# Performance work log

Measured on AMD Instinct MI355X. Metric: run time of the kernel, lower is better.

## Reference

```python
import jax, jax.numpy as jnp
import numpy as np
import math

B, S, D, H = 4, 2048, 768, 12
HD = D // H  # 64


def setup_inputs() -> dict:
    key = jax.random.key(0)
    ks = jax.random.split(key, 9)
    s = 0.02
    return {
        "hidden_states": jax.random.normal(ks[0], (B, S, D), jnp.float32),
        "layout_q": jax.random.normal(ks[1], (B, S, D), jnp.float32),
        "layout_k": jax.random.normal(ks[2], (B, S, D), jnp.float32),
        "attention_mask": jnp.zeros((B, 1, 1, S), jnp.float32),
        "Wq": jax.random.normal(ks[3], (D, D), jnp.float32) * s,
        "bq": jnp.zeros((D,), jnp.float32),
        "Wk": jax.random.normal(ks[4], (D, D), jnp.float32) * s,
        "bk": jnp.zeros((D,), jnp.float32),
        "Wv": jax.random.normal(ks[5], (D, D), jnp.float32) * s,
        "bv": jnp.zeros((D,), jnp.float32),
    }


def _split_heads(x):
    # [B,S,D] -> [B,H,S,HD]
    return x.reshape(B, S, H, HD).transpose(0, 2, 1, 3)


def reference(hidden_states, layout_q, layout_k, attention_mask, Wq, bq, Wk, bk, Wv, bv):
    q = _split_heads(hidden_states @ Wq.T + bq)
    k = _split_heads(hidden_states @ Wk.T + bk)
    v = _split_heads(hidden_states @ Wv.T + bv)
    lq = _split_heads(layout_q)
    lk = _split_heads(layout_k)
    scale = 1.0 / math.sqrt(HD)
    # dual-stream scores: content + layout, both [B,H,S,S]
    scores = (jnp.einsum("bhqd,bhkd->bhqk", q, k)
              + jnp.einsum("bhqd,bhkd->bhqk", lq, lk)) * scale
    scores = scores + attention_mask
    probs = jax.nn.softmax(scores, axis=-1)
    ctx = jnp.einsum("bhqk,bhkd->bhqd", probs, v)
    return ctx.transpose(0, 2, 1, 3).reshape(B, S, D)
```

## Files before the change

kernel.cpp:

```cpp
#include <hip/hip_runtime.h>


typedef __attribute__((ext_vector_type(8))) short short8;
typedef __attribute__((ext_vector_type(4))) float floatx4;

#define LOG2E 1.4426950408889634f
#define QSCL 0.18033688011112042f

static constexpr int Sn = 2048, Dn = 768, Hn = 12, BHn = 48;

__device__ __forceinline__ unsigned short f2bf(float f) {
  unsigned u = __float_as_uint(f);
  u += 0x7FFFu + ((u >> 16) & 1u);
  return (unsigned short)(u >> 16);
}

__device__ __forceinline__ unsigned pack2bf(float lo, float hi) {
  return (unsigned)f2bf(lo) | ((unsigned)f2bf(hi) << 16);
}

typedef const __attribute__((address_space(1))) unsigned int* gas_t;
typedef __attribute__((address_space(3))) unsigned int* las_t;
__device__ __forceinline__ void async16(const void* g, void* l) {
  __builtin_amdgcn_global_load_lds((gas_t)g, (las_t)l, 16, 0, 0);
}

__global__ void cast_hs_kernel(const float* __restrict__ in, unsigned short* __restrict__ out, int n4) {
  int i = blockIdx.x * 256 + threadIdx.x;
  if (i >= n4) return;
  float4 v = ((const float4*)in)[i];
  ushort4 o = make_ushort4(f2bf(v.x), f2bf(v.y), f2bf(v.z), f2bf(v.w));
  ((ushort4*)out)[i] = o;
}

__global__ void cast_w_kernel(const float* __restrict__ w0, const float* __restrict__ w1,
                              const float* __restrict__ w2, unsigned short* __restrict__ out) {
  int i = blockIdx.x * 256 + threadIdx.x;
  const float* src = (blockIdx.y == 0) ? w0 : (blockIdx.y == 1) ? w1 : w2;
  float4 v = ((const float4*)src)[i];
  ushort4 o = make_ushort4(f2bf(v.x), f2bf(v.y), f2bf(v.z), f2bf(v.w));
  ((ushort4*)(out + (size_t)blockIdx.y * Dn * Dn))[i] = o;
}

__global__ void pack_layout_kernel(const float* __restrict__ lq, const float* __restrict__ lk,
                                   unsigned short* __restrict__ Qc, unsigned short* __restrict__ Kc) {
  int idx = blockIdx.x * 256 + threadIdx.x;
  const float* src = blockIdx.y ? lk : lq;
  unsigned short* dst = blockIdx.y ? Kc : Qc;
  const float sc = blockIdx.y ? 1.0f : QSCL;
  int d8 = idx & 7;
  int tt = idx >> 3;
  int h = tt % Hn;
  int bs = tt / Hn;
  int b = bs >> 11, s = bs & (Sn - 1);
  float4 v0 = ((const float4*)src)[idx * 2];
  float4 v1 = ((const float4*)src)[idx * 2 + 1];
  short8 o;
  o[0] = (short)f2bf(v0.x * sc); o[1] = (short)f2bf(v0.y * sc);
  o[2] = (short)f2bf(v0.z * sc); o[3] = (short)f2bf(v0.w * sc);
  o[4] = (short)f2bf(v1.x * sc); o[5] = (short)f2bf(v1.y * sc);
  o[6] = (short)f2bf(v1.z * sc); o[7] = (short)f2bf(v1.w * sc);
  size_t off = ((size_t)(b * Hn + h) * Sn + s) * 128 + 64 + d8 * 8;
  *(short8*)(dst + off) = o;
}

__global__ __launch_bounds__(256, 3)
void proj_kernel(const unsigned short* __restrict__ X,
                 const unsigned short* __restrict__ Wb,
                 const float* __restrict__ bq, const float* __restrict__ bk, const float* __restrict__ bv,
                 unsigned short* __restrict__ Qc, unsigned short* __restrict__ Kc,
                 unsigned short* __restrict__ Vt) {
  __shared__ __align__(16) unsigned short sMem[16384];
  unsigned short* const sA = sMem;
  unsigned short* const sB = sMem + 8192;

  const int z = blockIdx.z;
  const unsigned short* W = Wb + (size_t)z * Dn * Dn;
  const float* bias = (z == 0) ? bq : (z == 1) ? bk : bv;

  const int t = threadIdx.x;
  const int lane = t & 63, wave = t >> 6;
  const int wm = wave >> 1, wn = wave & 1;
  const int quad = lane >> 4, col15 = lane & 15;
  const int m0 = blockIdx.y * 128, n0 = blockIdx.x * 128;

  const int srow = lane >> 3, schunk = lane & 7;

  floatx4 acc[4][4];
#pragma unroll
  for (int i = 0; i < 4; i++)
#pragma unroll
    for (int j = 0; j < 4; j++) acc[i][j] = (floatx4){0.f, 0.f, 0.f, 0.f};

  for (int k0 = 0; k0 < Dn; k0 += 64) {
    __syncthreads();
#pragma unroll
    for (int c = 0; c < 4; c++) {
      int row = wave * 32 + c * 8 + srow;
      int g = schunk ^ (row & 7);
      async16(X + (size_t)(m0 + row) * Dn + k0 + g * 8, sA + (wave * 32 + c * 8) * 64);
      async16(W + (size_t)(n0 + row) * Dn + k0 + g * 8, sB + (wave * 32 + c * 8) * 64);
    }
    __syncthreads();
#pragma unroll
    for (int kk = 0; kk < 2; kk++) {
      short8 af[4], bf[4];
      const int slot = ((kk * 4 + quad) ^ (col15 & 7)) * 8;
#pragma unroll
      for (int i = 0; i < 4; i++)
        af[i] = *(const short8*)(sA + (wm * 64 + i * 16 + col15) * 64 + slot);
#pragma unroll
      for (int j = 0; j < 4; j++)
        bf[j] = *(const short8*)(sB + (wn * 64 + j * 16 + col15) * 64 + slot);
#pragma unroll
      for (int i = 0; i < 4; i++)
#pragma unroll
        for (int j = 0; j < 4; j++)
          acc[i][j] = __builtin_amdgcn_mfma_f32_16x16x32_bf16(af[i], bf[j], acc[i][j], 0, 0, 0);
    }
  }

  __syncthreads();
  const int b = m0 >> 11;
  const int s0g = m0 & (Sn - 1);
  const int h0 = n0 >> 6;

  if (z < 2) {
    const float scl = (z == 0) ? QSCL : 1.0f;
    unsigned short* dst0 = (z == 0) ? Qc : Kc;
#pragma unroll
    for (int j = 0; j < 4; j++) {
      int nl = wn * 64 + j * 16 + col15;
      float bias_n = bias[n0 + nl];
#pragma unroll
      for (int i = 0; i < 4; i++) {
        int mb = wm * 64 + i * 16 + quad * 4;
#pragma unroll
        for (int r = 0; r < 4; r++) {
          int m = mb + r;
          sMem[m * 128 + (nl ^ (((m >> 2) & 3) << 4))] = f2bf((acc[i][j][r] + bias_n) * scl);
        }
      }
    }
    __syncthreads();
#pragma unroll
    for (int cc = 0; cc < 8; cc++) {
      int idx = cc * 256 + t;
      int m = idx >> 4, piece = idx & 15;
      int h = h0 + (piece >> 3), d8 = piece & 7;
      short8 v = *(const short8*)(sMem + m * 128 + (piece ^ (((m >> 2) & 3) << 1)) * 8);
      *(short8*)(dst0 + ((size_t)(b * Hn + h) * Sn + s0g + m) * 128 + d8 * 8) = v;
    }
  } else {
#pragma unroll
    for (int j = 0; j < 4; j++) {
      int nl = wn * 64 + j * 16 + col15;
      float bias_n = bias[n0 + nl];
#pragma unroll
      for (int i = 0; i < 4; i++) {
        int mb = wm * 64 + i * 16 + quad * 4;
        ushort4 pk = make_ushort4(f2bf(acc[i][j][0] + bias_n), f2bf(acc[i][j][1] + bias_n),
                                  f2bf(acc[i][j][2] + bias_n), f2bf(acc[i][j][3] + bias_n));
        *(ushort4*)(sMem + nl * 128 + (mb ^ ((nl & 7) << 4))) = pk;
      }
    }
    __syncthreads();
#pragma unroll
    for (int cc = 0; cc < 8; cc++) {
      int idx = cc * 256 + t;
      int nl = idx >> 4, piece = idx & 15;
      int h = h0 + (nl >> 6), d = nl & 63;
      short8 v = *(const short8*)(sMem + nl * 128 + (piece ^ ((nl & 7) << 1)) * 8);
      *(short8*)(Vt + ((size_t)(b * Hn + h) * 64 + d) * Sn + s0g + piece * 8) = v;
    }
  }
}

__global__ __launch_bounds__(256, 3)
void attn_kernel(const unsigned short* __restrict__ Qc,
                 const unsigned short* __restrict__ Kc,
                 const unsigned short* __restrict__ Vt,
                 const float* __restrict__ mask,
                 float* __restrict__ out) {
  __shared__ __align__(16) unsigned short sKc[64 * 128];
  __shared__ __align__(16) unsigned short sVt[64 * 64];
  __shared__ __align__(16) unsigned short sS[128 * 64];

  const int t = threadIdx.x;
  const int lane = t & 63, wave = t >> 6;
  const int quad = lane >> 4, col15 = lane & 15;
  const int swz = (col15 & 7) << 3;

  const int id = blockIdx.x;
  const int slot = id >> 3;
  const int bh = (id & 7) + 8 * (slot >> 4);
  const int q0 = (slot & 15) * 128;
  const int b = bh / Hn, h = bh % Hn;

  short8 aq[2][4];
  const unsigned short* Qbase = Qc + ((size_t)bh * Sn + q0) * 128;
#pragma unroll
  for (int i = 0; i < 2; i++)
#pragma unroll
    for (int kk = 0; kk < 4; kk++)
      aq[i][kk] = *(const short8*)(Qbase + (size_t)(wave * 32 + i * 16 + col15) * 128 + kk * 32 + quad * 8);

  floatx4 O[2][4], lacc[2];
#pragma unroll
  for (int i = 0; i < 2; i++) {
    lacc[i] = (floatx4){0.f, 0.f, 0.f, 0.f};
#pragma unroll
    for (int j = 0; j < 4; j++) O[i][j] = (floatx4){0.f, 0.f, 0.f, 0.f};
  }

  short8 aone;
  {
    short onev = (col15 == 0) ? (short)0x3F80 : (short)0;
#pragma unroll
    for (int e = 0; e < 8; e++) aone[e] = onev;
  }

  const unsigned short* Kbase = Kc + (size_t)bh * Sn * 128;
  const unsigned short* Vbase = Vt + (size_t)bh * 64 * Sn;
  const float* mbase = mask + (size_t)b * Sn;

  const int krow = lane >> 4, kslot = lane & 15;
  const int vrow = lane >> 3, vslot = lane & 7;

  for (int kt = 0; kt < Sn / 64; kt++) {
    __syncthreads();
#pragma unroll
    for (int c = 0; c < 4; c++) {
      int row = wave * 16 + c * 4 + krow;
      int g = (kslot & 8) | ((kslot ^ row) & 7);
      async16(Kbase + (size_t)(kt * 64 + row) * 128 + g * 8, sKc + (wave * 16 + c * 4) * 128);
    }
#pragma unroll
    for (int c = 0; c < 2; c++) {
      int row = wave * 16 + c * 8 + vrow;
      int g = vslot ^ (row & 7);
      async16(Vbase + (size_t)row * Sn + kt * 64 + g * 8, sVt + (wave * 16 + c * 8) * 64);
    }
    float m64 = mbase[kt * 64 + lane] * LOG2E;
    __syncthreads();
    const bool nomask = __all(m64 == 0.0f);

    floatx4 sacc[4][2];
#pragma unroll
    for (int jm = 0; jm < 4; jm++) {
      sacc[jm][0] = (floatx4){0.f, 0.f, 0.f, 0.f};
      sacc[jm][1] = (floatx4){0.f, 0.f, 0.f, 0.f};
    }
#pragma unroll
    for (int kk = 0; kk < 4; kk++) {
      const int slotK = (((kk * 4 + quad) & 8) | (((kk * 4 + quad) ^ col15) & 7)) * 8;
#pragma unroll
      for (int jm = 0; jm < 4; jm++) {
        short8 ak = *(const short8*)(sKc + (jm * 16 + col15) * 128 + slotK);
        sacc[jm][0] = __builtin_amdgcn_mfma_f32_16x16x32_bf16(ak, aq[0][kk], sacc[jm][0], 0, 0, 0);
        sacc[jm][1] = __builtin_amdgcn_mfma_f32_16x16x32_bf16(ak, aq[1][kk], sacc[jm][1], 0, 0, 0);
      }
    }

    float mvv[4][4];
    if (!nomask) {
#pragma unroll
      for (int jm = 0; jm < 4; jm++)
#pragma unroll
        for (int r = 0; r < 4; r++) mvv[jm][r] = __shfl(m64, jm * 16 + quad * 4 + r);
    }

#pragma unroll
    for (int iq = 0; iq < 2; iq++) {
      unsigned short* srow = sS + (wave * 32 + iq * 16 + col15) * 64;
#pragma unroll
      for (int jm = 0; jm < 4; jm++) {
        float p0 = sacc[jm][iq][0], p1 = sacc[jm][iq][1];
        float p2 = sacc[jm][iq][2], p3 = sacc[jm][iq][3];
        if (!nomask) { p0 += mvv[jm][0]; p1 += mvv[jm][1]; p2 += mvv[jm][2]; p3 += mvv[jm][3]; }
        p0 = __builtin_amdgcn_exp2f(p0); p1 = __builtin_amdgcn_exp2f(p1);
        p2 = __builtin_amdgcn_exp2f(p2); p3 = __builtin_amdgcn_exp2f(p3);
        uint2 w;
        w.x = pack2bf(p0, p1);
        w.y = pack2bf(p2, p3);
        *(uint2*)(srow + ((jm * 16 + quad * 4) ^ swz)) = w;
      }
    }

#pragma unroll
    for (int kk = 0; kk < 2; kk++) {
      short8 pb0 = *(const short8*)(sS + (wave * 32 + col15) * 64 + ((kk * 32 + quad * 8) ^ swz));
      short8 pb1 = *(const short8*)(sS + (wave * 32 + 16 + col15) * 64 + ((kk * 32 + quad * 8) ^ swz));
      const int slotV = ((kk * 4 + quad) ^ (col15 & 7)) * 8;
#pragma unroll
      for (int jd = 0; jd < 4; jd++) {
        short8 av = *(const short8*)(sVt + (jd * 16 + col15) * 64 + slotV);
        O[0][jd] = __builtin_amdgcn_mfma_f32_16x16x32_bf16(av, pb0, O[0][jd], 0, 0, 0);
        O[1][jd] = __builtin_amdgcn_mfma_f32_16x16x32_bf16(av, pb1, O[1][jd], 0, 0, 0);
      }
      lacc[0] = __builtin_amdgcn_mfma_f32_16x16x32_bf16(aone, pb0, lacc[0], 0, 0, 0);
      lacc[1] = __builtin_amdgcn_mfma_f32_16x16x32_bf16(aone, pb1, lacc[1], 0, 0, 0);
    }
  }

#pragma unroll
  for (int iq = 0; iq < 2; iq++) {
    float inv = 1.0f / __shfl(lacc[iq][0], col15);
    int qrow = q0 + wave * 32 + iq * 16 + col15;
    float* obase = out + ((size_t)b * Sn + qrow) * Dn + h * 64 + quad * 4;
#pragma unroll
    for (int jd = 0; jd < 4; jd++) {
      float4 o4 = make_float4(O[iq][jd][0] * inv, O[iq][jd][1] * inv,
                              O[iq][jd][2] * inv, O[iq][jd][3] * inv);
      *(float4*)(obase + jd * 16) = o4;
    }
  }
}

extern "C" void kernel_launch(void* const* d_in, const int* in_sizes, int n_in,
                              void* d_out, int out_size, void* d_ws, size_t ws_size,
                              hipStream_t stream) {
  const float* hs   = (const float*)d_in[0];
  const float* lq   = (const float*)d_in[1];
  const float* lk   = (const float*)d_in[2];
  const float* mask = (const float*)d_in[3];
  const float* Wq   = (const float*)d_in[4];
  const float* bq   = (const float*)d_in[5];
  const float* Wk   = (const float*)d_in[6];
  const float* bk   = (const float*)d_in[7];
  const float* Wv   = (const float*)d_in[8];
  const float* bv   = (const float*)d_in[9];
  float* out = (float*)d_out;

  char* ws = (char*)d_ws;
  unsigned short* Xbf = (unsigned short*)ws;
  unsigned short* Wbf = (unsigned short*)(ws + 12582912);
  unsigned short* Qc  = (unsigned short*)(ws + 12582912 + 3538944);
  unsigned short* Kc  = Qc + (size_t)BHn * Sn * 128;
  unsigned short* Vt  = Kc + (size_t)BHn * Sn * 128;

  cast_hs_kernel<<<6144, 256, 0, stream>>>(hs, Xbf, 1572864);
  cast_w_kernel<<<dim3(576, 3), 256, 0, stream>>>(Wq, Wk, Wv, Wbf);
  pack_layout_kernel<<<dim3(3072, 2), 256, 0, stream>>>(lq, lk, Qc, Kc);
  proj_kernel<<<dim3(6, 64, 3), 256, 0, stream>>>(Xbf, Wbf, bq, bk, bv, Qc, Kc, Vt);
  attn_kernel<<<768, 256, 0, stream>>>(Qc, Kc, Vt, mask, out);
}
```

Before: 293.7 us.

## Double-buffer K/V tiles in attention loop and raise MFMA wave priority

Adds double-buffered LDS for K and V so the next tile's async global-to-LDS loads are issued before computing on the current tile, with one barrier per iteration instead of two. The mask value for the next tile is also prefetched. MFMA sections are wrapped in s_setprio, and the bf16 pack of the probabilities switches from round-to-nearest to truncation, which slightly changes numerics. The larger LDS footprint lowers the occupancy target from 3 to 2 blocks per CU, trading parallelism for load/compute overlap.

```diff
diff --git a/kernel.cpp b/kernel.cpp
--- a/kernel.cpp
+++ b/kernel.cpp
@@ -13,10 +13,6 @@
   unsigned u = __float_as_uint(f);
   u += 0x7FFFu + ((u >> 16) & 1u);
   return (unsigned short)(u >> 16);
-}
-
-__device__ __forceinline__ unsigned pack2bf(float lo, float hi) {
-  return (unsigned)f2bf(lo) | ((unsigned)f2bf(hi) << 16);
 }
 
 typedef const __attribute__((address_space(1))) unsigned int* gas_t;
@@ -176,14 +172,14 @@
   }
 }
 
-__global__ __launch_bounds__(256, 3)
+__global__ __launch_bounds__(256, 2)
 void attn_kernel(const unsigned short* __restrict__ Qc,
                  const unsigned short* __restrict__ Kc,
                  const unsigned short* __restrict__ Vt,
                  const float* __restrict__ mask,
                  float* __restrict__ out) {
-  __shared__ __align__(16) unsigned short sKc[64 * 128];
-  __shared__ __align__(16) unsigned short sVt[64 * 64];
+  __shared__ __align__(16) unsigned short sK2[2][64 * 128];
+  __shared__ __align__(16) unsigned short sV2[2][64 * 64];
   __shared__ __align__(16) unsigned short sS[128 * 64];
 
   const int t = threadIdx.x;
@@ -227,23 +223,36 @@
   const int krow = lane >> 4, kslot = lane & 15;
   const int vrow = lane >> 3, vslot = lane & 7;
 
-  for (int kt = 0; kt < Sn / 64; kt++) {
-    __syncthreads();
+  auto stageKV = [&](int tile, int buf) {
+    unsigned short* sKn = &sK2[buf][0];
+    unsigned short* sVn = &sV2[buf][0];
 #pragma unroll
     for (int c = 0; c < 4; c++) {
       int row = wave * 16 + c * 4 + krow;
       int g = (kslot & 8) | ((kslot ^ row) & 7);
-      async16(Kbase + (size_t)(kt * 64 + row) * 128 + g * 8, sKc + (wave * 16 + c * 4) * 128);
+      async16(Kbase + (size_t)(tile * 64 + row) * 128 + g * 8, sKn + (wave * 16 + c * 4) * 128);
     }
 #pragma unroll
     for (int c = 0; c < 2; c++) {
       int row = wave * 16 + c * 8 + vrow;
       int g = vslot ^ (row & 7);
-      async16(Vbase + (size_t)row * Sn + kt * 64 + g * 8, sVt + (wave * 16 + c * 8) * 64);
-    }
-    float m64 = mbase[kt * 64 + lane] * LOG2E;
-    __syncthreads();
-    const bool nomask = __all(m64 == 0.0f);
+      async16(Vbase + (size_t)row * Sn + tile * 64 + g * 8, sVn + (wave * 16 + c * 8) * 64);
+    }
+  };
+
+  constexpr int NT = Sn / 64;
+  stageKV(0, 0);
+  float mcur = mbase[lane] * LOG2E;
+  __syncthreads();
+
+  for (int kt = 0; kt < NT; kt++) {
+    const int cur = kt & 1;
+    if (kt + 1 < NT) stageKV(kt + 1, cur ^ 1);
+    const int tn = (kt + 1 < NT) ? kt + 1 : NT - 1;
+    float mnew = mbase[tn * 64 + lane] * LOG2E;
+    const bool nomask = __all(mcur == 0.0f);
+    const unsigned short* sKcur = &sK2[cur][0];
+    const unsigned short* sVcur = &sV2[cur][0];
 
     floatx4 sacc[4][2];
 #pragma unroll
@@ -251,23 +260,25 @@
       sacc[jm][0] = (floatx4){0.f, 0.f, 0.f, 0.f};
       sacc[jm][1] = (floatx4){0.f, 0.f, 0.f, 0.f};
     }
+    __builtin_amdgcn_s_setprio(1);
 #pragma unroll
     for (int kk = 0; kk < 4; kk++) {
       const int slotK = (((kk * 4 + quad) & 8) | (((kk * 4 + quad) ^ col15) & 7)) * 8;
 #pragma unroll
       for (int jm = 0; jm < 4; jm++) {
-        short8 ak = *(const short8*)(sKc + (jm * 16 + col15) * 128 + slotK);
+        short8 ak = *(const short8*)(sKcur + (jm * 16 + col15) * 128 + slotK);
         sacc[jm][0] = __builtin_amdgcn_mfma_f32_16x16x32_bf16(ak, aq[0][kk], sacc[jm][0], 0, 0, 0);
         sacc[jm][1] = __builtin_amdgcn_mfma_f32_16x16x32_bf16(ak, aq[1][kk], sacc[jm][1], 0, 0, 0);
       }
     }
+    __builtin_amdgcn_s_setprio(0);
 
     float mvv[4][4];
     if (!nomask) {
 #pragma unroll
       for (int jm = 0; jm < 4; jm++)
 #pragma unroll
-        for (int r = 0; r < 4; r++) mvv[jm][r] = __shfl(m64, jm * 16 + quad * 4 + r);
+        for (int r = 0; r < 4; r++) mvv[jm][r] = __shfl(mcur, jm * 16 + quad * 4 + r);
     }
 
 #pragma unroll
@@ -281,12 +292,13 @@
         p0 = __builtin_amdgcn_exp2f(p0); p1 = __builtin_amdgcn_exp2f(p1);
         p2 = __builtin_amdgcn_exp2f(p2); p3 = __builtin_amdgcn_exp2f(p3);
         uint2 w;
-        w.x = pack2bf(p0, p1);
-        w.y = pack2bf(p2, p3);
+        w.x = (__float_as_uint(p0) >> 16) | (__float_as_uint(p1) & 0xFFFF0000u);
+        w.y = (__float_as_uint(p2) >> 16) | (__float_as_uint(p3) & 0xFFFF0000u);
         *(uint2*)(srow + ((jm * 16 + quad * 4) ^ swz)) = w;
       }
     }
 
+    __builtin_amdgcn_s_setprio(1);
 #pragma unroll
     for (int kk = 0; kk < 2; kk++) {
       short8 pb0 = *(const short8*)(sS + (wave * 32 + col15) * 64 + ((kk * 32 + quad * 8) ^ swz));
@@ -294,13 +306,17 @@
       const int slotV = ((kk * 4 + quad) ^ (col15 & 7)) * 8;
 #pragma unroll
       for (int jd = 0; jd < 4; jd++) {
-        short8 av = *(const short8*)(sVt + (jd * 16 + col15) * 64 + slotV);
+        short8 av = *(const short8*)(sVcur + (jd * 16 + col15) * 64 + slotV);
         O[0][jd] = __builtin_amdgcn_mfma_f32_16x16x32_bf16(av, pb0, O[0][jd], 0, 0, 0);
         O[1][jd] = __builtin_amdgcn_mfma_f32_16x16x32_bf16(av, pb1, O[1][jd], 0, 0, 0);
       }
       lacc[0] = __builtin_amdgcn_mfma_f32_16x16x32_bf16(aone, pb0, lacc[0], 0, 0, 0);
       lacc[1] = __builtin_amdgcn_mfma_f32_16x16x32_bf16(aone, pb1, lacc[1], 0, 0, 0);
     }
+    __builtin_amdgcn_s_setprio(0);
+
+    __syncthreads();
+    mcur = mnew;
   }
 
 #pragma unroll
```

Measured after the change: 316.2 us. 1.08x slower.
